# Kernel optimization log

Measured on AMD Instinct MI355X. Metric: run time of the kernel, lower is better.

Reference implementation:

```python
import jax, jax.numpy as jnp
import numpy as np

TOTAL_BITS = 16
FRAC_BITS = 8
SCALE = 2.0 ** FRAC_BITS
QMIN = -(2.0 ** (TOTAL_BITS - 1)) / SCALE
QMAX = (2.0 ** (TOTAL_BITS - 1) - 1) / SCALE


def quant(x):
    # fixed-point quantize: round to frac_bits, clamp to total_bits range (STE grad)
    q = jnp.clip(jnp.round(x * SCALE) / SCALE, QMIN, QMAX)
    return x + jax.lax.stop_gradient(q - x)


def hard_sigmoid(x):
    return jnp.clip(x / 6.0 + 0.5, 0.0, 1.0)


def hard_tanh(x):
    return jnp.clip(x, -1.0, 1.0)


def setup_inputs() -> dict:
    key = jax.random.key(0)
    ks = jax.random.split(key, 7)
    B, T, I, H, O = 256, 512, 128, 256, 1
    return {
        "x": jax.random.normal(ks[0], (B, T, I), jnp.float32),
        "w_ih": jax.random.normal(ks[1], (4 * H, I), jnp.float32) * 0.05,
        "w_hh": jax.random.normal(ks[2], (4 * H, H), jnp.float32) * 0.05,
        "b_ih": jax.random.normal(ks[3], (4 * H,), jnp.float32) * 0.05,
        "b_hh": jax.random.normal(ks[4], (4 * H,), jnp.float32) * 0.05,
        "w_lin": jax.random.normal(ks[5], (O, H), jnp.float32) * 0.05,
        "b_lin": jax.random.normal(ks[6], (O,), jnp.float32) * 0.05,
    }


def reference(x, w_ih, w_hh, b_ih, b_hh, w_lin, b_lin):
    B, T, I = x.shape
    H = w_hh.shape[1]
    xq = quant(x)
    w_ih_q, w_hh_q = quant(w_ih), quant(w_hh)
    b_ih_q, b_hh_q = quant(b_ih), quant(b_hh)
    # input projection for all timesteps at once: [B,T,4H]
    gi = quant(jnp.einsum("bti,gi->btg", xq, w_ih_q) + b_ih_q)

    def step(carry, gi_t):
        h, c = carry
        gh = quant(h @ w_hh_q.T + b_hh_q)
        g = quant(gi_t + gh)
        i_g, f_g, c_g, o_g = jnp.split(g, 4, axis=-1)
        i_g = quant(hard_sigmoid(i_g))
        f_g = quant(hard_sigmoid(f_g))
        c_g = quant(hard_tanh(c_g))
        o_g = quant(hard_sigmoid(o_g))
        c_new = quant(quant(f_g * c) + quant(i_g * c_g))
        h_new = quant(o_g * quant(hard_tanh(c_new)))
        return (h_new, c_new), None

    h0 = jnp.zeros((B, H), x.dtype)
    c0 = jnp.zeros((B, H), x.dtype)
    (h_last, _), _ = jax.lax.scan(step, (h0, c0), jnp.swapaxes(gi, 0, 1))
    # x[:, -1] of the LSTM output == h_last; fixed-point linear head
    return quant(h_last @ quant(w_lin).T + quant(b_lin))
```

## Files before the change

kernel.cpp:

```cpp
#include <hip/hip_runtime.h>
#include <stdint.h>
#include <stddef.h>

typedef int i32x4 __attribute__((ext_vector_type(4)));
typedef int i32x2 __attribute__((ext_vector_type(2)));

#define WS_WFRAG   0u
#define WS_WIH     262144u
#define WS_BIASHH  393216u
#define WS_BIASIH  397312u
#define WS_WLIN    401408u
#define WS_BLIN    402432u
#define WS_HSTATE  409600u
#define WS_CSTATE  540672u
#define WS_GI      1064960u

#define MFMA_I8(a,b,c) __builtin_amdgcn_mfma_i32_16x16x64_i8(a,b,c,0,0,0)
#define RHE8(x) ((((x) + 127) + (((x) >> 8) & 1)) >> 8)

#define DPPX1(v) __builtin_amdgcn_update_dpp(0, (v), 0xB1, 0xF, 0xF, true)
#define DPPX2(v) __builtin_amdgcn_update_dpp(0, (v), 0x4E, 0xF, 0xF, true)

#define BAR() do { asm volatile("s_waitcnt lgkmcnt(0)" ::: "memory"); \
                   __builtin_amdgcn_s_barrier(); } while (0)

__device__ __forceinline__ float clamp3(float x, float lo, float hi) {
    return __builtin_amdgcn_fmed3f(x, lo, hi);
}
__device__ __forceinline__ float q16f(float x) {
    return clamp3(__builtin_rintf(x * 256.0f), -32768.0f, 32767.0f);
}
__device__ __forceinline__ int iclamp(int v, int lo, int hi) {
    return v < lo ? lo : (v > hi ? hi : v);
}
__device__ __forceinline__ int sigq(int u) {
    int q = __mul24(u, 43691) >> 18;
    int r = u - __mul24(q, 6);
    return q + (((r + (q & 1)) > 3) ? 1 : 0);
}

__global__ void prep_kernel(const float* __restrict__ wih, const float* __restrict__ whh,
                            const float* __restrict__ bih, const float* __restrict__ bhh,
                            const float* __restrict__ wlin, const float* __restrict__ blin,
                            uint8_t* __restrict__ ws) {
    int tid = blockIdx.x * blockDim.x + threadIdx.x;
    {
        int p = tid;
        int j = p & 15, lane = (p >> 4) & 63, ks = (p >> 10) & 3, t8 = (p >> 12) & 7, w = (p >> 15) & 7;
        int row = (t8 >> 1) * 256 + w * 32 + (t8 & 1) * 16 + (lane & 15);
        int k = ks * 64 + (lane >> 4) * 16 + j;
        int v = (int)q16f(whh[row * 256 + k]);
        v = iclamp(v, -127, 127);
        ((int8_t*)(ws + WS_WFRAG))[p] = (int8_t)v;
    }
    if (tid < 131072) {
        int gcol = tid >> 7, k = tid & 127;
        int v = (int)q16f(wih[gcol * 128 + k]);
        v = iclamp(v, -127, 127);
        ((int8_t*)(ws + WS_WIH))[tid] = (int8_t)v;
    }
    if (tid < 1024) {
        ((int*)(ws + WS_BIASHH))[tid] = ((int)q16f(bhh[tid])) * 256;
        ((int*)(ws + WS_BIASIH))[tid] = ((int)q16f(bih[tid])) * 256;
    }
    if (tid < 256) ((int*)(ws + WS_WLIN))[tid] = (int)q16f(wlin[tid]);
    if (tid == 0)  ((int*)(ws + WS_BLIN))[0]   = (int)q16f(blin[0]);
}

__launch_bounds__(512, 2)
__global__ void gi_kernel(const float* __restrict__ x, uint8_t* __restrict__ ws, int t0) {
    __shared__ uint8_t xa[2048], xb[2048];
    int tid = threadIdx.x;
    int wgr = blockIdx.x;
    int tl  = blockIdx.y;
    int t   = t0 + tl;
    {
        int row = tid >> 5, c4 = (tid & 31) * 4;
        int b = wgr * 16 + row;
        const float4 xv = *(const float4*)(x + ((size_t)b * 512 + t) * 128 + c4);
        int v0 = (int)q16f(xv.x), v1 = (int)q16f(xv.y), v2 = (int)q16f(xv.z), v3 = (int)q16f(xv.w);
        uint32_t da = ((uint32_t)((v0 >> 7) & 255)) | ((uint32_t)((v1 >> 7) & 255) << 8) |
                      ((uint32_t)((v2 >> 7) & 255) << 16) | ((uint32_t)((v3 >> 7) & 255) << 24);
        uint32_t db = ((uint32_t)(v0 & 127)) | ((uint32_t)(v1 & 127) << 8) |
                      ((uint32_t)(v2 & 127) << 16) | ((uint32_t)(v3 & 127) << 24);
        int addr = row * 128 + (((c4 >> 4) ^ (row & 7)) * 16) + (c4 & 15);
        *(uint32_t*)(xa + addr) = da;
        *(uint32_t*)(xb + addr) = db;
    }
    __syncthreads();
    int wid = tid >> 6, lane = tid & 63, lr = lane & 15, lg = lane >> 4;
    const uint8_t* wq = ws + WS_WIH;
    i32x4 af[8][2];
#pragma unroll
    for (int mt = 0; mt < 8; ++mt) {
        int gcol = (mt >> 1) * 256 + wid * 32 + (mt & 1) * 16 + lr;
#pragma unroll
        for (int kt = 0; kt < 2; ++kt)
            af[mt][kt] = *(const i32x4*)(wq + gcol * 128 + kt * 64 + lg * 16);
    }
    i32x4 bha[2], bhb[2];
#pragma unroll
    for (int kt = 0; kt < 2; ++kt) {
        int addr = lr * 128 + ((((kt * 4) + lg) ^ (lr & 7)) * 16);
        bha[kt] = *(const i32x4*)(xa + addr);
        bhb[kt] = *(const i32x4*)(xb + addr);
    }
    i32x4 acch[8], accl[8];
    const int* bi = (const int*)(ws + WS_BIASIH);
#pragma unroll
    for (int mt = 0; mt < 8; ++mt) {
        i32x4 z = {0, 0, 0, 0};
        int gb = (mt >> 1) * 256 + wid * 32 + (mt & 1) * 16 + lg * 4;
        i32x4 bc = *(const i32x4*)(bi + gb);
        acch[mt] = MFMA_I8(af[mt][0], bha[0], z);
        accl[mt] = MFMA_I8(af[mt][0], bhb[0], bc);
        acch[mt] = MFMA_I8(af[mt][1], bha[1], acch[mt]);
        accl[mt] = MFMA_I8(af[mt][1], bhb[1], accl[mt]);
    }
    int gq[8][4];
#pragma unroll
    for (int mt = 0; mt < 8; ++mt)
#pragma unroll
        for (int rr = 0; rr < 4; ++rr) {
            int v = acch[mt][rr] * 128 + accl[mt][rr];
            gq[mt][rr] = iclamp(RHE8(v), -32768, 32767);
        }
    unsigned batch = (unsigned)(wgr * 16 + lr);
#pragma unroll
    for (int mm2 = 0; mm2 < 2; ++mm2)
#pragma unroll
        for (int rr2 = 0; rr2 < 4; ++rr2) {
            i32x2 outv;
            outv[0] = (gq[mm2][rr2] & 0xFFFF)     | (gq[4 + mm2][rr2] << 16);
            outv[1] = (gq[2 + mm2][rr2] & 0xFFFF) | (gq[6 + mm2][rr2] << 16);
            int Lp = ((rr2 & 1) << 1) | (mm2 << 2) | ((rr2 >> 1) << 3) | (lg << 4);
            *(i32x2*)(ws + WS_GI + (size_t)tl * 524288u +
                      (size_t)((batch * 8u + (unsigned)wid) * 64u + (unsigned)Lp) * 4u) = outv;
        }
}

__launch_bounds__(512, 2)
__global__ void recur_kernel(uint8_t* __restrict__ ws, float* __restrict__ out, int t0, int cs) {
    __shared__ __align__(16) uint8_t hbuf[2][512];
    __shared__ long long redl[8];
    int tid = threadIdx.x, w = tid >> 6, lane = tid & 63;
    int wb = blockIdx.x;
    int gsel = lane & 1;
    int cp   = (lane >> 1) & 1;
    int mm   = (lane >> 2) & 1;
    int X    = (lane >> 3) & 1;
    int sg   = lane >> 4;
    uint8_t* hb0 = &hbuf[0][0];

    i32x4 wf[8][4];
#pragma unroll
    for (int t8 = 0; t8 < 8; ++t8)
#pragma unroll
        for (int ks = 0; ks < 4; ++ks)
            wf[t8][ks] = *(const i32x4*)(ws + WS_WFRAG + (((unsigned)(w * 8 + t8) * 4 + ks) << 10) + lane * 16);

    int addrB[4];
#pragma unroll
    for (int ks = 0; ks < 4; ++ks)
        addrB[ks] = cp * 256 + ks * 64 + sg * 16;

    int k_own = w * 32 + mm * 16 + sg * 4 + 2 * X + cp;
    int addrW = (gsel ? 256 : 0) + k_own;
    int biasP[2], wlv;
    {
        const int* bhh256 = (const int*)(ws + WS_BIASHH);
        int G0 = gsel, G1 = gsel + 2;
        biasP[0] = bhh256[G0 * 256 + k_own] + 768 * 256;
        biasP[1] = bhh256[G1 * 256 + k_own] + (G1 == 2 ? 0 : 768 * 256);
        wlv = ((const int*)(ws + WS_WLIN))[k_own];
    }
    size_t gioff = (size_t)((unsigned)wb * 8u + (unsigned)w) * 256u + (unsigned)lane * 4u;

    uint8_t* hst = ws + WS_HSTATE + (unsigned)wb * 512u;
    int* cst = (int*)(ws + WS_CSTATE) + (unsigned)wb * 512u + (unsigned)tid;

    int c_;
    if (t0 == 0) {
        c_ = 0;
        if (tid < 128) *(uint32_t*)(hb0 + tid * 4) = 0u;
    } else {
        c_ = *cst;
        if (tid < 128) *(uint32_t*)(hb0 + tid * 4) = *(const uint32_t*)(hst + tid * 4);
    }
    int gcur = *(const int*)(ws + WS_GI + gioff);
    int gnx;
    __syncthreads();

    int hl_ = 0;
    const i32x4 zerov = {0, 0, 0, 0};

#define PLANEPAIR(T0, T1, T2, T3, U, V)                                                \
    int U, V;                                                                          \
    {                                                                                  \
        int ua = X ? acc[T0][2] : acc[T0][0], va = X ? acc[T0][3] : acc[T0][1];        \
        int ub = X ? acc[T1][2] : acc[T1][0], vb = X ? acc[T1][3] : acc[T1][1];        \
        int uc = X ? acc[T2][2] : acc[T2][0], vc = X ? acc[T2][3] : acc[T2][1];        \
        int ud = X ? acc[T3][2] : acc[T3][0], vd = X ? acc[T3][3] : acc[T3][1];        \
        int u0 = mm ? ub : ua, v0 = mm ? vb : va;                                      \
        int u1 = mm ? ud : uc, v1 = mm ? vd : vc;                                      \
        U = gsel ? u1 : u0;                                                            \
        V = gsel ? v1 : v0;                                                            \
    }
#define SLOT(U, V, BIAS, OUTG)                                                         \
    int OUTG;                                                                          \
    {                                                                                  \
        int own = cp ? V : U;                                                          \
        int snd = cp ? U : V;                                                          \
        int z = DPPX2(snd);                                                            \
        int hi = cp ? z : own;                                                         \
        int lo = cp ? own : z;                                                         \
        OUTG = RHE8(hi * 4 + lo + (BIAS));                                             \
    }
#define STEP(PP, GUSE, GPRE, TPRE)                                                     \
    {                                                                                  \
        GPRE = *(const int*)(ws + WS_GI + (size_t)(TPRE) * 524288u + gioff);           \
        i32x4 acc[8];                                                                  \
        _Pragma("unroll")                                                              \
        for (int ks = 0; ks < 4; ++ks) {                                               \
            i32x4 bf = *(const i32x4*)(hb0 + (PP) * 512 + addrB[ks]);                  \
            _Pragma("unroll")                                                          \
            for (int t8 = 0; t8 < 8; ++t8)                                             \
                acc[t8] = (ks == 0) ? MFMA_I8(wf[t8][0], bf, zerov)                    \
                                    : MFMA_I8(wf[t8][ks], bf, acc[t8]);                \
        }                                                                              \
        PLANEPAIR(0, 1, 2, 3, uA, vA)                                                  \
        PLANEPAIR(4, 5, 6, 7, uB, vB)                                                  \
        SLOT(uA, vA, biasP[0], gA)                                                     \
        SLOT(uB, vB, biasP[1], gB)                                                     \
        int givlo = ((GUSE) << 16) >> 16, givhi = (GUSE) >> 16;                        \
        int first = sigq(iclamp(gA + givlo, 0, 1536));         \
        int sigB  = sigq(iclamp(gB + givhi, 0, 1536));                                 \
        int clpB  = iclamp(gB + givhi, -256, 256);                      \
        int second = gsel ? sigB : clpB;                       \
        int z1 = DPPX1(first);                                                         \
        int z2 = DPPX1(second);                                                        \
        int i_g = gsel ? z1 : first;                                                   \
        int f_g = gsel ? first : z1;                                                   \
        int c_g = gsel ? z2 : second;                                                  \
        int o_g = gsel ? second : z2;                                                  \
        int fcq = RHE8(__mul24(f_g, c_));                                              \
        int icq = RHE8(__mul24(i_g, c_g));                                             \
        int cn  = iclamp(fcq + icq, -32768, 32767);                                    \
        c_ = cn;                                                                       \
        int th = iclamp(cn, -256, 256);                                                \
        int hq = RHE8(__mul24(o_g, th));                                               \
        *(int8_t*)(hb0 + ((PP) ^ 1) * 512 + addrW) = (int8_t)(gsel ? (hq & 3) : (hq >> 2)); \
        hl_ = hq;                                                                      \
        BAR();                                                                         \
    }

    for (int tl = 0; tl < cs; tl += 2) {
        int tn2 = (tl + 2 < cs) ? tl + 2 : 0;
        STEP(0, gcur, gnx, tl + 1)
        STEP(1, gnx, gcur, tn2)
    }
#undef STEP
#undef SLOT
#undef PLANEPAIR

    if (tid < 128) *(uint32_t*)(hst + tid * 4) = *(const uint32_t*)(hb0 + tid * 4);
    *cst = c_;

    if (t0 + cs == 512) {
        long long s = gsel ? 0LL : (long long)hl_ * (long long)wlv;
        s += __shfl_xor(s, 1);
        s += __shfl_xor(s, 2);
        s += __shfl_xor(s, 4);
        s += __shfl_xor(s, 8);
        s += __shfl_xor(s, 16);
        s += __shfl_xor(s, 32);
        if (lane == 0) redl[w] = s;
        __syncthreads();
        if (tid == 0) {
            long long tot = 0;
#pragma unroll
            for (int ww = 0; ww < 8; ++ww) tot += redl[ww];
            tot += 256LL * (long long)((const int*)(ws + WS_BLIN))[0];
            long long q = ((tot + 127) + ((tot >> 8) & 1)) >> 8;
            q = q < -32768 ? -32768 : (q > 32767 ? 32767 : q);
            out[wb] = (float)q * 0.00390625f;
        }
    }
}

extern "C" void kernel_launch(void* const* d_in, const int* in_sizes, int n_in,
                              void* d_out, int out_size, void* d_ws, size_t ws_size,
                              hipStream_t stream) {
    const float* x    = (const float*)d_in[0];
    const float* wih  = (const float*)d_in[1];
    const float* whh  = (const float*)d_in[2];
    const float* bih  = (const float*)d_in[3];
    const float* bhh  = (const float*)d_in[4];
    const float* wlin = (const float*)d_in[5];
    const float* blin = (const float*)d_in[6];
    float* out = (float*)d_out;
    uint8_t* ws = (uint8_t*)d_ws;

    prep_kernel<<<512, 512, 0, stream>>>(wih, whh, bih, bhh, wlin, blin, ws);

    int cs = 512;
    while ((size_t)WS_GI + (size_t)cs * 524288u > ws_size && cs > 8) cs >>= 1;

    for (int t0 = 0; t0 < 512; t0 += cs) {
        gi_kernel<<<dim3(16, cs), 512, 0, stream>>>(x, ws, t0);
        recur_kernel<<<256, 512, 0, stream>>>(ws, out, t0, cs);
    }
}
```

Baseline: 576.5 us.

## Process four timesteps per gi block and pack h-state bytes into dword LDS stores

The input-projection kernel now handles four timesteps per block. Weight fragments and biases are loaded once and reused across those steps, and x staging is double-buffered in LDS. In the recurrent kernel, the per-lane byte stores of the quantized hidden state are combined with DPP shuffles into one 32-bit LDS store per four lanes, with a matching change to the B-fragment read layout. The aim is to cut redundant weight loads and LDS store traffic on the serial critical path, at the cost of extra DPP ops and a per-iteration barrier in gi_kernel.

```diff
diff --git a/kernel.cpp b/kernel.cpp
--- a/kernel.cpp
+++ b/kernel.cpp
@@ -18,8 +18,9 @@
 #define MFMA_I8(a,b,c) __builtin_amdgcn_mfma_i32_16x16x64_i8(a,b,c,0,0,0)
 #define RHE8(x) ((((x) + 127) + (((x) >> 8) & 1)) >> 8)
 
-#define DPPX1(v) __builtin_amdgcn_update_dpp(0, (v), 0xB1, 0xF, 0xF, true)
-#define DPPX2(v) __builtin_amdgcn_update_dpp(0, (v), 0x4E, 0xF, 0xF, true)
+#define DPPX1(v)   __builtin_amdgcn_update_dpp(0, (v), 0xB1, 0xF, 0xF, true)
+#define DPPX2(v)   __builtin_amdgcn_update_dpp(0, (v), 0x4E, 0xF, 0xF, true)
+#define DPPROR8(v) __builtin_amdgcn_update_dpp(0, (v), 0x128, 0xF, 0xF, true)
 
 #define BAR() do { asm volatile("s_waitcnt lgkmcnt(0)" ::: "memory"); \
                    __builtin_amdgcn_s_barrier(); } while (0)
@@ -69,74 +70,89 @@
 
 __launch_bounds__(512, 2)
 __global__ void gi_kernel(const float* __restrict__ x, uint8_t* __restrict__ ws, int t0) {
-    __shared__ uint8_t xa[2048], xb[2048];
+    __shared__ uint8_t xa[2][2048], xb[2][2048];
     int tid = threadIdx.x;
     int wgr = blockIdx.x;
-    int tl  = blockIdx.y;
-    int t   = t0 + tl;
-    {
+    int tlb = blockIdx.y * 4;
+    int wid = tid >> 6, lane = tid & 63, lr = lane & 15, lg = lane >> 4;
+
+    const uint8_t* wq = ws + WS_WIH;
+    i32x4 af[8][2];
+#pragma unroll
+    for (int mt = 0; mt < 8; ++mt) {
+        int gcol = (mt >> 1) * 256 + wid * 32 + (mt & 1) * 16 + lr;
+#pragma unroll
+        for (int kt = 0; kt < 2; ++kt)
+            af[mt][kt] = *(const i32x4*)(wq + gcol * 128 + kt * 64 + lg * 16);
+    }
+    i32x4 bcv[8];
+    const int* bi = (const int*)(ws + WS_BIASIH);
+#pragma unroll
+    for (int mt = 0; mt < 8; ++mt) {
+        int gb = (mt >> 1) * 256 + wid * 32 + (mt & 1) * 16 + lg * 4;
+        bcv[mt] = *(const i32x4*)(bi + gb);
+    }
+
+    auto STAGE = [&](int tl, int buf) {
         int row = tid >> 5, c4 = (tid & 31) * 4;
         int b = wgr * 16 + row;
-        const float4 xv = *(const float4*)(x + ((size_t)b * 512 + t) * 128 + c4);
+        const float4 xv = *(const float4*)(x + ((size_t)b * 512 + (t0 + tl)) * 128 + c4);
         int v0 = (int)q16f(xv.x), v1 = (int)q16f(xv.y), v2 = (int)q16f(xv.z), v3 = (int)q16f(xv.w);
         uint32_t da = ((uint32_t)((v0 >> 7) & 255)) | ((uint32_t)((v1 >> 7) & 255) << 8) |
                       ((uint32_t)((v2 >> 7) & 255) << 16) | ((uint32_t)((v3 >> 7) & 255) << 24);
         uint32_t db = ((uint32_t)(v0 & 127)) | ((uint32_t)(v1 & 127) << 8) |
                       ((uint32_t)(v2 & 127) << 16) | ((uint32_t)(v3 & 127) << 24);
         int addr = row * 128 + (((c4 >> 4) ^ (row & 7)) * 16) + (c4 & 15);
-        *(uint32_t*)(xa + addr) = da;
-        *(uint32_t*)(xb + addr) = db;
-    }
+        *(uint32_t*)(&xa[buf][0] + addr) = da;
+        *(uint32_t*)(&xb[buf][0] + addr) = db;
+    };
+
+    STAGE(tlb, 0);
     __syncthreads();
-    int wid = tid >> 6, lane = tid & 63, lr = lane & 15, lg = lane >> 4;
-    const uint8_t* wq = ws + WS_WIH;
-    i32x4 af[8][2];
-#pragma unroll
-    for (int mt = 0; mt < 8; ++mt) {
-        int gcol = (mt >> 1) * 256 + wid * 32 + (mt & 1) * 16 + lr;
-#pragma unroll
-        for (int kt = 0; kt < 2; ++kt)
-            af[mt][kt] = *(const i32x4*)(wq + gcol * 128 + kt * 64 + lg * 16);
-    }
-    i32x4 bha[2], bhb[2];
-#pragma unroll
-    for (int kt = 0; kt < 2; ++kt) {
-        int addr = lr * 128 + ((((kt * 4) + lg) ^ (lr & 7)) * 16);
-        bha[kt] = *(const i32x4*)(xa + addr);
-        bhb[kt] = *(const i32x4*)(xb + addr);
-    }
-    i32x4 acch[8], accl[8];
-    const int* bi = (const int*)(ws + WS_BIASIH);
-#pragma unroll
-    for (int mt = 0; mt < 8; ++mt) {
-        i32x4 z = {0, 0, 0, 0};
-        int gb = (mt >> 1) * 256 + wid * 32 + (mt & 1) * 16 + lg * 4;
-        i32x4 bc = *(const i32x4*)(bi + gb);
-        acch[mt] = MFMA_I8(af[mt][0], bha[0], z);
-        accl[mt] = MFMA_I8(af[mt][0], bhb[0], bc);
-        acch[mt] = MFMA_I8(af[mt][1], bha[1], acch[mt]);
-        accl[mt] = MFMA_I8(af[mt][1], bhb[1], accl[mt]);
-    }
-    int gq[8][4];
-#pragma unroll
-    for (int mt = 0; mt < 8; ++mt)
-#pragma unroll
-        for (int rr = 0; rr < 4; ++rr) {
-            int v = acch[mt][rr] * 128 + accl[mt][rr];
-            gq[mt][rr] = iclamp(RHE8(v), -32768, 32767);
+
+    for (int s4 = 0; s4 < 4; ++s4) {
+        int tl = tlb + s4;
+        if (s4 < 3) STAGE(tl + 1, (s4 + 1) & 1);
+        int buf = s4 & 1;
+
+        i32x4 bha[2], bhb[2];
+#pragma unroll
+        for (int kt = 0; kt < 2; ++kt) {
+            int addr = lr * 128 + ((((kt * 4) + lg) ^ (lr & 7)) * 16);
+            bha[kt] = *(const i32x4*)(&xa[buf][0] + addr);
+            bhb[kt] = *(const i32x4*)(&xb[buf][0] + addr);
         }
-    unsigned batch = (unsigned)(wgr * 16 + lr);
-#pragma unroll
-    for (int mm2 = 0; mm2 < 2; ++mm2)
-#pragma unroll
-        for (int rr2 = 0; rr2 < 4; ++rr2) {
-            i32x2 outv;
-            outv[0] = (gq[mm2][rr2] & 0xFFFF)     | (gq[4 + mm2][rr2] << 16);
-            outv[1] = (gq[2 + mm2][rr2] & 0xFFFF) | (gq[6 + mm2][rr2] << 16);
-            int Lp = ((rr2 & 1) << 1) | (mm2 << 2) | ((rr2 >> 1) << 3) | (lg << 4);
-            *(i32x2*)(ws + WS_GI + (size_t)tl * 524288u +
-                      (size_t)((batch * 8u + (unsigned)wid) * 64u + (unsigned)Lp) * 4u) = outv;
+        i32x4 acch[8], accl[8];
+#pragma unroll
+        for (int mt = 0; mt < 8; ++mt) {
+            i32x4 z = {0, 0, 0, 0};
+            acch[mt] = MFMA_I8(af[mt][0], bha[0], z);
+            accl[mt] = MFMA_I8(af[mt][0], bhb[0], bcv[mt]);
+            acch[mt] = MFMA_I8(af[mt][1], bha[1], acch[mt]);
+            accl[mt] = MFMA_I8(af[mt][1], bhb[1], accl[mt]);
         }
+        int gq[8][4];
+#pragma unroll
+        for (int mt = 0; mt < 8; ++mt)
+#pragma unroll
+            for (int rr = 0; rr < 4; ++rr) {
+                int v = acch[mt][rr] * 128 + accl[mt][rr];
+                gq[mt][rr] = iclamp(RHE8(v), -32768, 32767);
+            }
+        unsigned batch = (unsigned)(wgr * 16 + lr);
+#pragma unroll
+        for (int mm2 = 0; mm2 < 2; ++mm2)
+#pragma unroll
+            for (int rr2 = 0; rr2 < 4; ++rr2) {
+                i32x2 outv;
+                outv[0] = (gq[mm2][rr2] & 0xFFFF)     | (gq[4 + mm2][rr2] << 16);
+                outv[1] = (gq[2 + mm2][rr2] & 0xFFFF) | (gq[6 + mm2][rr2] << 16);
+                int Lp = ((rr2 & 1) << 1) | (mm2 << 2) | ((rr2 >> 1) << 3) | (lg << 4);
+                *(i32x2*)(ws + WS_GI + (size_t)tl * 524288u +
+                          (size_t)((batch * 8u + (unsigned)wid) * 64u + (unsigned)Lp) * 4u) = outv;
+            }
+        __syncthreads();
+    }
 }
 
 __launch_bounds__(512, 2)
@@ -162,10 +178,10 @@
     int addrB[4];
 #pragma unroll
     for (int ks = 0; ks < 4; ++ks)
-        addrB[ks] = cp * 256 + ks * 64 + sg * 16;
+        addrB[ks] = ks * 128 + cp * 64 + sg * 16;
 
     int k_own = w * 32 + mm * 16 + sg * 4 + 2 * X + cp;
-    int addrW = (gsel ? 256 : 0) + k_own;
+    int addrW4 = (w >> 1) * 128 + gsel * 64 + ((w & 1) * 2 + mm) * 16 + sg * 4;
     int biasP[2], wlv;
     {
         const int* bhh256 = (const int*)(ws + WS_BIASHH);
@@ -249,7 +265,13 @@
         c_ = cn;                                                                       \
         int th = iclamp(cn, -256, 256);                                                \
         int hq = RHE8(__mul24(o_g, th));                                               \
-        *(int8_t*)(hb0 + ((PP) ^ 1) * 512 + addrW) = (int8_t)(gsel ? (hq & 3) : (hq >> 2)); \
+               \
+        unsigned hby = (unsigned)(gsel ? (hq & 3) : (hq >> 2)) & 255u;                 \
+        unsigned pv = hby << (8 * (2 * X + cp));                                       \
+        pv |= (unsigned)DPPX2((int)pv);                                                \
+        pv |= (unsigned)DPPROR8((int)pv);                                              \
+        if ((lane & 10) == 0)                                                          \
+            *(uint32_t*)(hb0 + ((PP) ^ 1) * 512 + addrW4) = pv;                        \
         hl_ = hq;                                                                      \
         BAR();                                                                         \
     }
@@ -307,7 +329,7 @@
     while ((size_t)WS_GI + (size_t)cs * 524288u > ws_size && cs > 8) cs >>= 1;
 
     for (int t0 = 0; t0 < 512; t0 += cs) {
-        gi_kernel<<<dim3(16, cs), 512, 0, stream>>>(x, ws, t0);
+        gi_kernel<<<dim3(16, cs / 4), 512, 0, stream>>>(x, ws, t0);
         recur_kernel<<<256, 512, 0, stream>>>(ws, out, t0, cs);
     }
 }
```

Result: faster. 529.0 us (-8.2%).
